# Optimization experiments

Measured on AMD Instinct MI355X. Metric: run time of the kernel, lower is better.

## Reference

```python
import jax, jax.numpy as jnp
import numpy as np

B = 1048576  # batch size
EPS_CLAMP_LO = 1e-6
EPS_CLAMP_HI = 1.0 - 1e-6


def _build_mask():
    # mask[k, i, j] = 1 iff i + j == k, flattened to [19, 100]
    i = np.arange(10)
    m = np.zeros((19, 10, 10), dtype=np.float32)
    ii, jj = np.meshgrid(i, i, indexing='ij')
    m[(ii + jj).ravel(), ii.ravel(), jj.ravel()] = 1.0
    return jnp.asarray(m.reshape(19, 100))


def setup_inputs() -> dict:
    key = jax.random.key(0)
    k1, k2, k3, k4 = jax.random.split(key, 4)
    # concept probabilities: uniform then normalize rows to sum 1
    p1 = jax.random.uniform(k1, (B, 10), dtype=jnp.float32)
    p1 = p1 / p1.sum(axis=1, keepdims=True)
    p2 = jax.random.uniform(k2, (B, 10), dtype=jnp.float32)
    p2 = p2 / p2.sum(axis=1, keepdims=True)
    # learnable permutation-tree weights (binaryTreeLogicNet leaf maps)
    W1 = jax.random.uniform(k3, (10, 10), dtype=jnp.float32)
    W2 = jax.random.uniform(k4, (10, 10), dtype=jnp.float32)
    mask = _build_mask()
    return {"p1": p1, "p2": p2, "W1": W1, "W2": W2, "mask": mask}


def _minmax_norm(W):
    lo = W.min(axis=1, keepdims=True)
    hi = W.max(axis=1, keepdims=True)
    return (W - lo) / (hi - lo + 1e-8)


def reference(p1, p2, W1, W2, mask):
    # input_to_leaf: learned soft permutation with minmax-normalized weights
    p1p = p1 @ _minmax_norm(W1)                      # [B,10]
    p2p = p2 @ _minmax_norm(W2)                      # [B,10]
    # MinMaxAggregator graded AND at andness=1.0 -> elementwise min over all pairs
    s = jnp.minimum(p1p[:, :, None], p2p[:, None, :])  # [B,10,10]
    one_minus = 1.0 - jnp.clip(s, EPS_CLAMP_LO, EPS_CLAMP_HI)
    log_one_minus = jnp.log(one_minus + 1e-12).reshape(-1, 100)  # [B,100]
    # fused masked reduction over all 19 sum bins: [B,100] @ [100,19]
    log_prod = log_one_minus @ mask.T                # [B,19]
    y_prob = 1.0 - jnp.exp(log_prod)                 # smooth OR per sum class
    y_prob = y_prob / (y_prob.sum(axis=1, keepdims=True) + 1e-9)
    return y_prob
```

## Files before the change

kernel.cpp:

```cpp
#include <hip/hip_runtime.h>


#define NBLOCKS 1024
#define PANELS 4

__global__ __launch_bounds__(256, 4) void bacon_main(
    const float* __restrict__ p1, const float* __restrict__ p2,
    const float* __restrict__ W1, const float* __restrict__ W2,
    float* __restrict__ out)
{
    __shared__ __align__(16) float s_out[2][4864];
    __shared__ __align__(16) float s_w[240];

    const int t = threadIdx.x;
    const int blk = blockIdx.x;
    const size_t row0 = (size_t)blk * (256 * PANELS) + t;

    float2 va[2][5], vb[2][5];
    {
        const float2* g1 = (const float2*)(p1 + row0 * 10);
        const float2* g2 = (const float2*)(p2 + row0 * 10);
        #pragma unroll
        for (int e = 0; e < 5; ++e) { va[0][e] = g1[e]; vb[0][e] = g2[e]; }
    }

    if (t < 20) {
        const float* row = ((t < 10) ? W1 : W2) + (t % 10) * 10;
        float r[10];
        #pragma unroll
        for (int i = 0; i < 10; ++i) r[i] = row[i];
        float lo = r[0], hi = r[0];
        #pragma unroll
        for (int i = 1; i < 10; ++i) {
            lo = fminf(lo, r[i]);
            hi = fmaxf(hi, r[i]);
        }
        float inv = 1.0f / (hi - lo + 1e-8f);
        float* o = s_w + ((t < 10) ? 0 : 120) + (t % 10) * 12;
        #pragma unroll
        for (int i = 0; i < 10; ++i) o[i] = (r[i] - lo) * inv;
        o[10] = 0.0f; o[11] = 0.0f;
    }
    __syncthreads();

    #pragma unroll
    for (int p = 0; p < PANELS; ++p) {
        const int cur = p & 1;

        if (p + 1 < PANELS) {
            const int nxt = cur ^ 1;
            const float2* g1 = (const float2*)(p1 + (row0 + (size_t)(p + 1) * 256) * 10);
            const float2* g2 = (const float2*)(p2 + (row0 + (size_t)(p + 1) * 256) * 10);
            #pragma unroll
            for (int e = 0; e < 5; ++e) { va[nxt][e] = g1[e]; vb[nxt][e] = g2[e]; }
        }

        float A[10], Bv[10];
        #pragma unroll
        for (int i = 0; i < 10; ++i) { A[i] = 1.0f; Bv[i] = 1.0f; }
        #pragma unroll
        for (int k = 0; k < 10; ++k) {
            const float ak = (k & 1) ? va[cur][k >> 1].y : va[cur][k >> 1].x;
            const float bk = (k & 1) ? vb[cur][k >> 1].y : vb[cur][k >> 1].x;
            const float4* w1q = (const float4*)(s_w + k * 12);
            const float4* w2q = (const float4*)(s_w + 120 + k * 12);
            float4 u0 = w1q[0], u1 = w1q[1];
            float2 u2 = *(const float2*)(s_w + k * 12 + 8);
            float4 v0 = w2q[0], v1 = w2q[1];
            float2 v2 = *(const float2*)(s_w + 120 + k * 12 + 8);
            A[0] = fmaf(-ak, u0.x, A[0]); A[1] = fmaf(-ak, u0.y, A[1]);
            A[2] = fmaf(-ak, u0.z, A[2]); A[3] = fmaf(-ak, u0.w, A[3]);
            A[4] = fmaf(-ak, u1.x, A[4]); A[5] = fmaf(-ak, u1.y, A[5]);
            A[6] = fmaf(-ak, u1.z, A[6]); A[7] = fmaf(-ak, u1.w, A[7]);
            A[8] = fmaf(-ak, u2.x, A[8]); A[9] = fmaf(-ak, u2.y, A[9]);
            Bv[0] = fmaf(-bk, v0.x, Bv[0]); Bv[1] = fmaf(-bk, v0.y, Bv[1]);
            Bv[2] = fmaf(-bk, v0.z, Bv[2]); Bv[3] = fmaf(-bk, v0.w, Bv[3]);
            Bv[4] = fmaf(-bk, v1.x, Bv[4]); Bv[5] = fmaf(-bk, v1.y, Bv[5]);
            Bv[6] = fmaf(-bk, v1.z, Bv[6]); Bv[7] = fmaf(-bk, v1.w, Bv[7]);
            Bv[8] = fmaf(-bk, v2.x, Bv[8]); Bv[9] = fmaf(-bk, v2.y, Bv[9]);
        }

        float prod[19];
        #pragma unroll
        for (int k = 0; k < 19; ++k) prod[k] = 1.0f;
        #pragma unroll
        for (int i = 0; i < 10; ++i) {
            #pragma unroll
            for (int j = 0; j < 10; ++j) {
                prod[i + j] *= fmaxf(A[i], Bv[j]);
            }
        }

        float y[19];
        float tot = 0.0f;
        #pragma unroll
        for (int k = 0; k < 19; ++k) { y[k] = 1.0f - prod[k]; tot += y[k]; }
        float invn = __builtin_amdgcn_rcpf(tot + 1e-9f);

        #pragma unroll
        for (int k = 0; k < 19; ++k) s_out[cur][t * 19 + k] = y[k] * invn;
        __syncthreads();

        {
            const float4* so = (const float4*)s_out[cur];
            float4* go = (float4*)(out + ((size_t)blk * PANELS + p) * 4864);
            #pragma unroll
            for (int it = 0; it < 5; ++it) {
                int idx = t + it * 256;
                if (idx < 1216) go[idx] = so[idx];
            }
        }
    }
}

extern "C" void kernel_launch(void* const* d_in, const int* in_sizes, int n_in,
                              void* d_out, int out_size, void* d_ws, size_t ws_size,
                              hipStream_t stream) {
    const float* p1 = (const float*)d_in[0];
    const float* p2 = (const float*)d_in[1];
    const float* W1 = (const float*)d_in[2];
    const float* W2 = (const float*)d_in[3];
    bacon_main<<<NBLOCKS, 256, 0, stream>>>(p1, p2, W1, W2, (float*)d_out);
}
```

Before: 154.0 us.

## Use packed FMA for leaf maps, nontemporal output stores, and sched barriers

Rewrites the 10x10 leaf-map FMAs as 2-wide vector FMAs so the compiler can emit packed fp32 FMA instructions. Output copies from LDS to global become nontemporal stores to reduce cache pollution. Adds scheduling barriers after the prefetch loads so they are issued early, and drops the occupancy hint in the launch bounds. Together these aim to cut ALU issue count and memory-side overhead, at the cost of possibly different register allocation and occupancy.

After: 156.5 us. Within noise of the previous version (+1.6%).

```diff
diff --git a/kernel.cpp b/kernel.cpp
--- a/kernel.cpp
+++ b/kernel.cpp
@@ -1,28 +1,34 @@
 #include <hip/hip_runtime.h>
 
 
+typedef float v2f __attribute__((ext_vector_type(2)));
+typedef float v4f __attribute__((ext_vector_type(4)));
+
 #define NBLOCKS 1024
+#define TPB 256
 #define PANELS 4
 
-__global__ __launch_bounds__(256, 4) void bacon_main(
+__global__ __launch_bounds__(TPB) void bacon_main(
     const float* __restrict__ p1, const float* __restrict__ p2,
     const float* __restrict__ W1, const float* __restrict__ W2,
     float* __restrict__ out)
 {
-    __shared__ __align__(16) float s_out[2][4864];
+    __shared__ __align__(16) float s_out[2][TPB * 19];
     __shared__ __align__(16) float s_w[240];
 
     const int t = threadIdx.x;
     const int blk = blockIdx.x;
-    const size_t row0 = (size_t)blk * (256 * PANELS) + t;
+    const size_t blk_row0 = (size_t)blk * (PANELS * TPB);
 
     float2 va[2][5], vb[2][5];
+
     {
-        const float2* g1 = (const float2*)(p1 + row0 * 10);
-        const float2* g2 = (const float2*)(p2 + row0 * 10);
+        const float2* g1 = (const float2*)(p1 + (blk_row0 + t) * 10);
+        const float2* g2 = (const float2*)(p2 + (blk_row0 + t) * 10);
         #pragma unroll
         for (int e = 0; e < 5; ++e) { va[0][e] = g1[e]; vb[0][e] = g2[e]; }
     }
+    __builtin_amdgcn_sched_barrier(0);
 
     if (t < 20) {
         const float* row = ((t < 10) ? W1 : W2) + (t % 10) * 10;
@@ -49,35 +55,47 @@
 
         if (p + 1 < PANELS) {
             const int nxt = cur ^ 1;
-            const float2* g1 = (const float2*)(p1 + (row0 + (size_t)(p + 1) * 256) * 10);
-            const float2* g2 = (const float2*)(p2 + (row0 + (size_t)(p + 1) * 256) * 10);
+            const float2* g1 = (const float2*)(p1 + (blk_row0 + (size_t)(p + 1) * TPB + t) * 10);
+            const float2* g2 = (const float2*)(p2 + (blk_row0 + (size_t)(p + 1) * TPB + t) * 10);
             #pragma unroll
             for (int e = 0; e < 5; ++e) { va[nxt][e] = g1[e]; vb[nxt][e] = g2[e]; }
+            __builtin_amdgcn_sched_barrier(0);
         }
 
-        float A[10], Bv[10];
+        float a[10], b[10];
         #pragma unroll
-        for (int i = 0; i < 10; ++i) { A[i] = 1.0f; Bv[i] = 1.0f; }
+        for (int e = 0; e < 5; ++e) {
+            a[2 * e] = va[cur][e].x; a[2 * e + 1] = va[cur][e].y;
+            b[2 * e] = vb[cur][e].x; b[2 * e + 1] = vb[cur][e].y;
+        }
+
+        v2f A2[5], B2[5];
+        #pragma unroll
+        for (int m = 0; m < 5; ++m) { A2[m] = (v2f){1.0f, 1.0f}; B2[m] = (v2f){1.0f, 1.0f}; }
         #pragma unroll
         for (int k = 0; k < 10; ++k) {
-            const float ak = (k & 1) ? va[cur][k >> 1].y : va[cur][k >> 1].x;
-            const float bk = (k & 1) ? vb[cur][k >> 1].y : vb[cur][k >> 1].x;
             const float4* w1q = (const float4*)(s_w + k * 12);
             const float4* w2q = (const float4*)(s_w + 120 + k * 12);
             float4 u0 = w1q[0], u1 = w1q[1];
             float2 u2 = *(const float2*)(s_w + k * 12 + 8);
             float4 v0 = w2q[0], v1 = w2q[1];
             float2 v2 = *(const float2*)(s_w + 120 + k * 12 + 8);
-            A[0] = fmaf(-ak, u0.x, A[0]); A[1] = fmaf(-ak, u0.y, A[1]);
-            A[2] = fmaf(-ak, u0.z, A[2]); A[3] = fmaf(-ak, u0.w, A[3]);
-            A[4] = fmaf(-ak, u1.x, A[4]); A[5] = fmaf(-ak, u1.y, A[5]);
-            A[6] = fmaf(-ak, u1.z, A[6]); A[7] = fmaf(-ak, u1.w, A[7]);
-            A[8] = fmaf(-ak, u2.x, A[8]); A[9] = fmaf(-ak, u2.y, A[9]);
-            Bv[0] = fmaf(-bk, v0.x, Bv[0]); Bv[1] = fmaf(-bk, v0.y, Bv[1]);
-            Bv[2] = fmaf(-bk, v0.z, Bv[2]); Bv[3] = fmaf(-bk, v0.w, Bv[3]);
-            Bv[4] = fmaf(-bk, v1.x, Bv[4]); Bv[5] = fmaf(-bk, v1.y, Bv[5]);
-            Bv[6] = fmaf(-bk, v1.z, Bv[6]); Bv[7] = fmaf(-bk, v1.w, Bv[7]);
-            Bv[8] = fmaf(-bk, v2.x, Bv[8]); Bv[9] = fmaf(-bk, v2.y, Bv[9]);
+            v2f uw[5] = { {u0.x, u0.y}, {u0.z, u0.w}, {u1.x, u1.y}, {u1.z, u1.w}, {u2.x, u2.y} };
+            v2f vw[5] = { {v0.x, v0.y}, {v0.z, v0.w}, {v1.x, v1.y}, {v1.z, v1.w}, {v2.x, v2.y} };
+            const v2f na = (v2f){-a[k], -a[k]};
+            const v2f nb = (v2f){-b[k], -b[k]};
+            #pragma unroll
+            for (int m = 0; m < 5; ++m) {
+                A2[m] = __builtin_elementwise_fma(na, uw[m], A2[m]);
+                B2[m] = __builtin_elementwise_fma(nb, vw[m], B2[m]);
+            }
+        }
+
+        float A[10], Bv[10];
+        #pragma unroll
+        for (int m = 0; m < 5; ++m) {
+            A[2 * m] = A2[m].x;  A[2 * m + 1] = A2[m].y;
+            Bv[2 * m] = B2[m].x; Bv[2 * m + 1] = B2[m].y;
         }
 
         float prod[19];
@@ -102,12 +120,13 @@
         __syncthreads();
 
         {
-            const float4* so = (const float4*)s_out[cur];
-            float4* go = (float4*)(out + ((size_t)blk * PANELS + p) * 4864);
+            const v4f* so = (const v4f*)s_out[cur];
+            v4f* go = (v4f*)out + (size_t)(blk * PANELS + p) * 1216;
             #pragma unroll
             for (int it = 0; it < 5; ++it) {
-                int idx = t + it * 256;
-                if (idx < 1216) go[idx] = so[idx];
+                int idx = t + it * TPB;
+                if (idx < 1216)
+                    __builtin_nontemporal_store(so[idx], go + idx);
             }
         }
     }
@@ -120,5 +139,5 @@
     const float* p2 = (const float*)d_in[1];
     const float* W1 = (const float*)d_in[2];
     const float* W2 = (const float*)d_in[3];
-    bacon_main<<<NBLOCKS, 256, 0, stream>>>(p1, p2, W1, W2, (float*)d_out);
+    bacon_main<<<NBLOCKS, TPB, 0, stream>>>(p1, p2, W1, W2, (float*)d_out);
 }
```
